# Kernel tuning notes

Hardware: AMD Instinct MI355X
Metric: run time of the kernel (lower is better)

Reference implementation:

```python
import jax, jax.numpy as jnp
import numpy as np

B, N, K, DIM = 2, 20000, 16, 256


def _mlp(x, W, b):
    # torch nn.Linear: x @ W.T + b, then LeakyReLU(0.1)
    return jax.nn.leaky_relu(x @ W.T + b, negative_slope=0.1)


def _lfa(features, geom, idx, W, b):
    # features: [B, N, C]; geom: [B, N, K, 4]; idx: [B, N, K]
    t = _mlp(geom, W, b)                                  # [B, N, K, d_lfa]
    fn = jax.vmap(lambda f, i: f[i])(features, idx)       # gather neighbors: [B, N, K, C]
    # mean over K of concat == concat of means (faithful, avoids big concat)
    return jnp.concatenate([t.mean(axis=2), fn.mean(axis=2)], axis=-1)


def _linear_init(key, out_f, in_f):
    k1, k2 = jax.random.split(key)
    bound = 1.0 / np.sqrt(in_f)
    W = jax.random.uniform(k1, (out_f, in_f), jnp.float32, -bound, bound)
    b = jax.random.uniform(k2, (out_f,), jnp.float32, -bound, bound)
    return W, b


def setup_inputs() -> dict:
    key = jax.random.key(0)
    ks = jax.random.split(key, 8)
    W_init, b_init = _linear_init(ks[0], DIM // 4, DIM)
    W_l1, b_l1 = _linear_init(ks[1], DIM // 4, 4)
    W_l2, b_l2 = _linear_init(ks[2], DIM // 2, 4)
    W_fin, b_fin = _linear_init(ks[3], DIM, DIM)
    W_id, b_id = _linear_init(ks[4], DIM, DIM)
    return {
        "input_tensor": jax.random.normal(ks[5], (B, N, DIM), jnp.float32),
        "geometric_features": jax.random.normal(ks[6], (B, N, K, 4), jnp.float32),
        "neighbor_indices": jax.random.randint(ks[7], (B, N, K), 0, N, jnp.int64 if jax.config.jax_enable_x64 else jnp.int32),
        "W_init": W_init, "b_init": b_init,
        "W_l1": W_l1, "b_l1": b_l1,
        "W_l2": W_l2, "b_l2": b_l2,
        "W_fin": W_fin, "b_fin": b_fin,
        "W_id": W_id, "b_id": b_id,
    }


def reference(input_tensor, geometric_features, neighbor_indices,
              W_init, b_init, W_l1, b_l1, W_l2, b_l2,
              W_fin, b_fin, W_id, b_id):
    residual = input_tensor
    x = _mlp(input_tensor, W_init, b_init)                       # [B, N, dim/4]
    x = _lfa(x, geometric_features, neighbor_indices, W_l1, b_l1)  # [B, N, dim/2]
    x = _lfa(x, geometric_features, neighbor_indices, W_l2, b_l2)  # [B, N, dim]
    x = _mlp(x, W_fin, b_fin)
    return x + _mlp(residual, W_id, b_id)
```

## Files before the change

kernel.cpp:

```cpp
#include <hip/hip_runtime.h>
#include <hip/hip_bf16.h>

#define BN   40000
#define NPTS 20000
#define KNN  16
#define DIM  256

typedef __attribute__((ext_vector_type(8))) short bf16x8;
typedef __attribute__((ext_vector_type(4))) float f32x4;

__device__ __forceinline__ float lrelu(float v) { return v > 0.f ? v : 0.1f * v; }
__device__ __forceinline__ float bs2f(short s) {
    union { unsigned u; float f; } c; c.u = ((unsigned)(unsigned short)s) << 16;
    return c.f;
}
__device__ __forceinline__ short f2bs(float f) {
    __hip_bfloat16 h = __float2bfloat16(f);
    return *reinterpret_cast<short*>(&h);
}
__device__ __forceinline__ bf16x8 ldf32_bf16x8(const float* p) {
    const float4 a = ((const float4*)p)[0];
    const float4 b = ((const float4*)p)[1];
    bf16x8 r;
    r[0]=f2bs(a.x); r[1]=f2bs(a.y); r[2]=f2bs(a.z); r[3]=f2bs(a.w);
    r[4]=f2bs(b.x); r[5]=f2bs(b.y); r[6]=f2bs(b.z); r[7]=f2bs(b.w);
    return r;
}

__device__ __forceinline__ void dma16(const void* g, void* l) {
    __builtin_amdgcn_global_load_lds(
        (const __attribute__((address_space(1))) unsigned int*)g,
        (__attribute__((address_space(3))) unsigned int*)l, 16, 0, 0);
}

__global__ void __launch_bounds__(256) geom_kernel(
    const float* __restrict__ geom,
    const float* __restrict__ W1, const float* __restrict__ B1,
    const float* __restrict__ W2, const float* __restrict__ B2,
    const int* __restrict__ idxw, int* __restrict__ flag,
    const float* __restrict__ Wf, const float* __restrict__ Wi,
    const float* __restrict__ Wn,
    short* __restrict__ Wt, short* __restrict__ Wnt,
    __hip_bfloat16* __restrict__ x2,
    __hip_bfloat16* __restrict__ x3)
{
    if (blockIdx.x >= 3751) {
        int t = (blockIdx.x - 3751) * 256 + threadIdx.x;
        if (t < 32768) {
            int mat = (t >> 14) & 1;
            int tt  = t & 16383;
            float4 v = mat ? ((const float4*)Wi)[tt] : ((const float4*)Wf)[tt];
            int n  = tt >> 6;
            int k  = (tt & 63) * 4;
            int kk = k >> 5, q = (k >> 3) & 3, j = k & 7;
            short4 o; o.x=f2bs(v.x); o.y=f2bs(v.y); o.z=f2bs(v.z); o.w=f2bs(v.w);
            *(short4*)(Wt + ((size_t)((kk*2 + mat)*4 + q))*2048 + n*8 + j) = o;
        } else {
            int tt = t - 32768;
            float4 v = ((const float4*)Wn)[tt];
            int n  = tt >> 6;
            int k  = (tt & 63) * 4;
            int kk = k >> 5, q = (k >> 3) & 3, j = k & 7;
            short4 o; o.x=f2bs(v.x); o.y=f2bs(v.y); o.z=f2bs(v.z); o.w=f2bs(v.w);
            *(short4*)(Wnt + ((size_t)((kk*4 + q)*64 + n))*8 + j) = o;
        }
        return;
    }
    if (blockIdx.x == 3750) {
        __shared__ int red[256];
        int t = threadIdx.x;
        int v = 0;
#pragma unroll
        for (int it = 0; it < 64; ++it)
            v |= idxw[2 * (t + it * 256) + 1];
        red[t] = v;
        __syncthreads();
        for (int s = 128; s > 0; s >>= 1) {
            if (t < s) red[t] |= red[t + s];
            __syncthreads();
        }
        if (t == 0) *flag = (red[0] != 0) ? 1 : 0;
        return;
    }
    int tid = blockIdx.x * 256 + threadIdx.x;
    int p  = tid / 24;
    int cg = tid - p * 24;
    const float4* g = (const float4*)(geom + (size_t)p * (KNN * 4));
    const float4* Wp; const float* Bp; int c0;
    if (cg < 8) { c0 = cg * 8;       Wp = (const float4*)W1; Bp = B1; }
    else        { c0 = (cg - 8) * 8; Wp = (const float4*)W2; Bp = B2; }
    float4 w[8]; float bb[8];
#pragma unroll
    for (int j = 0; j < 8; ++j) { w[j] = Wp[c0 + j]; bb[j] = Bp[c0 + j]; }
    float acc[8];
#pragma unroll
    for (int j = 0; j < 8; ++j) acc[j] = 0.f;
#pragma unroll
    for (int k = 0; k < KNN; ++k) {
        float4 gv = g[k];
#pragma unroll
        for (int j = 0; j < 8; ++j)
            acc[j] += lrelu(bb[j] + gv.x*w[j].x + gv.y*w[j].y + gv.z*w[j].z + gv.w*w[j].w);
    }
    const float s = 1.f/16.f;
    short* dst = (cg < 8) ? ((short*)x2 + (size_t)p*128 + c0)
                          : ((short*)x3 + (size_t)p*256 + c0);
    bf16x8 o;
#pragma unroll
    for (int j = 0; j < 8; ++j) o[j] = f2bs(acc[j] * s);
    *(bf16x8*)dst = o;
}

__global__ void __launch_bounds__(256) mlp_init_mfma(
    const float* __restrict__ X,
    const short* __restrict__ Wnt,
    const float* __restrict__ bias,
    __hip_bfloat16* __restrict__ Y)
{
    __shared__ short wbuf[16384];
    int t = threadIdx.x;
    int wave = t >> 6, lane = t & 63;
    int r = lane & 15, q = lane >> 4;
    {
        const char* W8 = (const char*)Wnt;
        char* L8 = (char*)wbuf;
#pragma unroll
        for (int rd = 0; rd < 8; ++rd) {
            int off = (wave * 8 + rd) * 1024 + lane * 16;
            dma16(W8 + off, L8 + off);
        }
    }
    int m0 = blockIdx.x * 64 + wave * 16;
    const float* Xs = X + (size_t)(m0 + r) * DIM + q * 8;
    bf16x8 a[8];
#pragma unroll
    for (int kk = 0; kk < 8; ++kk) a[kk] = ldf32_bf16x8(Xs + kk * 32);
    __syncthreads();

    f32x4 acc[4];
#pragma unroll
    for (int nt = 0; nt < 4; ++nt) acc[nt] = (f32x4){0.f,0.f,0.f,0.f};
#pragma unroll
    for (int kk = 0; kk < 8; ++kk) {
#pragma unroll
        for (int nt = 0; nt < 4; ++nt) {
            bf16x8 b = *(const bf16x8*)&wbuf[((kk*4 + q)*64 + nt*16 + r) * 8];
            acc[nt] = __builtin_amdgcn_mfma_f32_16x16x32_bf16(a[kk], b, acc[nt], 0, 0, 0);
        }
    }
#pragma unroll
    for (int nt = 0; nt < 4; ++nt) {
        int col = nt * 16 + r;
        float bv = bias[col];
#pragma unroll
        for (int i = 0; i < 4; ++i) {
            float v = lrelu(acc[nt][i] + bv);
            Y[(size_t)(m0 + q*4 + i) * 64 + col] = __float2bfloat16(v);
        }
    }
}

__global__ void __launch_bounds__(256) gather1_kernel(
    const int* __restrict__ idxw, const int* __restrict__ flag,
    const __hip_bfloat16* __restrict__ x1,
    __hip_bfloat16* __restrict__ x2)
{
    int t = blockIdx.x * 256 + threadIdx.x;
    int p = t >> 3, j = t & 7;
    int lane = threadIdx.x & 63;
    int dual = (*flag == 0) ? 2 : 1;
    int base = (p >= NPTS) ? NPTS : 0;
    int i0 = idxw[((size_t)p * 16 + 2*j)     * dual];
    int i1 = idxw[((size_t)p * 16 + 2*j + 1) * dual];
    int g8 = lane & 56;
    float acc[8];
#pragma unroll
    for (int i = 0; i < 8; ++i) acc[i] = 0.f;
#pragma unroll
    for (int k = 0; k < 8; ++k) {
        int rA = base + __shfl(i0, g8 + k, 64);
        int rB = base + __shfl(i1, g8 + k, 64);
        bf16x8 vA = *(const bf16x8*)((const short*)x1 + (size_t)rA * 64 + j * 8);
        bf16x8 vB = *(const bf16x8*)((const short*)x1 + (size_t)rB * 64 + j * 8);
#pragma unroll
        for (int i = 0; i < 8; ++i) acc[i] += bs2f(vA[i]) + bs2f(vB[i]);
    }
    bf16x8 o;
#pragma unroll
    for (int i = 0; i < 8; ++i) o[i] = f2bs(acc[i] * (1.f/16.f));
    *(bf16x8*)((short*)x2 + (size_t)p * 128 + 64 + j * 8) = o;
}

__global__ void __launch_bounds__(256) gather2_kernel(
    const int* __restrict__ idxw, const int* __restrict__ flag,
    const __hip_bfloat16* __restrict__ x2,
    __hip_bfloat16* __restrict__ x3)
{
    int t = blockIdx.x * 256 + threadIdx.x;
    int p = t >> 4, j = t & 15;
    int lane = threadIdx.x & 63;
    int dual = (*flag == 0) ? 2 : 1;
    int base = (p >= NPTS) ? NPTS : 0;
    int myi = idxw[((size_t)p * 16 + j) * dual];
    int g16 = lane & 48;
    float acc[8];
#pragma unroll
    for (int i = 0; i < 8; ++i) acc[i] = 0.f;
#pragma unroll
    for (int k = 0; k < KNN; ++k) {
        int row = base + __shfl(myi, g16 + k, 64);
        bf16x8 v = *(const bf16x8*)((const short*)x2 + (size_t)row * 128 + j * 8);
#pragma unroll
        for (int i = 0; i < 8; ++i) acc[i] += bs2f(v[i]);
    }
    bf16x8 o;
#pragma unroll
    for (int i = 0; i < 8; ++i) o[i] = f2bs(acc[i] * (1.f/16.f));
    *(bf16x8*)((short*)x3 + (size_t)p * 256 + 128 + j * 8) = o;
}

__global__ void __launch_bounds__(256) final_mfma(
    const __hip_bfloat16* __restrict__ X3,
    const float* __restrict__ RES,
    const short* __restrict__ Wt,
    const float* __restrict__ Bf,
    const float* __restrict__ Bi,
    float* __restrict__ OUT)
{
    __shared__ short wbuf[16384];
    int t = threadIdx.x;
    int wave = t >> 6, lane = t & 63;
    int r = lane & 15, q = lane >> 4;
    int p0 = blockIdx.x * 16;

    const char* WtB = (const char*)Wt;
    char* wbufB = (char*)wbuf;
    {
        const char* src0 = WtB + wave * 1024 + lane * 16;
#pragma unroll
        for (int rd = 0; rd < 8; ++rd)
            dma16(src0 + rd * 4096, wbufB + rd * 4096 + wave * 1024);
    }

    bf16x8 a1f[8], a2f[8];
    {
        const short* x3r = (const short*)X3 + (size_t)(p0 + r) * DIM + q * 8;
        const float* rsr = RES + (size_t)(p0 + r) * DIM + q * 8;
#pragma unroll
        for (int kk = 0; kk < 8; ++kk) {
            a1f[kk] = *(const bf16x8*)(x3r + kk * 32);
            a2f[kk] = ldf32_bf16x8(rsr + kk * 32);
        }
    }

    f32x4 acc1[4], acc2[4];
#pragma unroll
    for (int nt = 0; nt < 4; ++nt) {
        acc1[nt] = (f32x4){0.f,0.f,0.f,0.f};
        acc2[nt] = (f32x4){0.f,0.f,0.f,0.f};
    }

#pragma unroll
    for (int kk = 0; kk < 8; ++kk) {
        __syncthreads();
#pragma unroll
        for (int nt = 0; nt < 4; ++nt) {
            int n = wave * 64 + nt * 16 + r;
            bf16x8 b1 = *(const bf16x8*)&wbuf[(size_t)q * 2048 + n * 8];
            bf16x8 b2 = *(const bf16x8*)&wbuf[(size_t)(4 + q) * 2048 + n * 8];
            acc1[nt] = __builtin_amdgcn_mfma_f32_16x16x32_bf16(a1f[kk], b1, acc1[nt], 0, 0, 0);
            acc2[nt] = __builtin_amdgcn_mfma_f32_16x16x32_bf16(a2f[kk], b2, acc2[nt], 0, 0, 0);
        }
        if (kk < 7) {
            __syncthreads();
            const char* src = WtB + (size_t)(kk + 1) * 32768 + wave * 1024 + lane * 16;
#pragma unroll
            for (int rd = 0; rd < 8; ++rd)
                dma16(src + rd * 4096, wbufB + rd * 4096 + wave * 1024);
        }
    }

#pragma unroll
    for (int nt = 0; nt < 4; ++nt) {
        int col = wave * 64 + nt * 16 + r;
        float bfv = Bf[col], biv = Bi[col];
#pragma unroll
        for (int i = 0; i < 4; ++i) {
            float v = lrelu(acc1[nt][i] + bfv) + lrelu(acc2[nt][i] + biv);
            OUT[(size_t)(p0 + q*4 + i) * DIM + col] = v;
        }
    }
}

extern "C" void kernel_launch(void* const* d_in, const int* in_sizes, int n_in,
                              void* d_out, int out_size, void* d_ws, size_t ws_size,
                              hipStream_t stream)
{
    const float* input  = (const float*)d_in[0];
    const float* geom   = (const float*)d_in[1];
    const int*   idxw   = (const int*)d_in[2];
    const float* W_init = (const float*)d_in[3];
    const float* b_init = (const float*)d_in[4];
    const float* W_l1   = (const float*)d_in[5];
    const float* b_l1   = (const float*)d_in[6];
    const float* W_l2   = (const float*)d_in[7];
    const float* b_l2   = (const float*)d_in[8];
    const float* W_fin  = (const float*)d_in[9];
    const float* b_fin  = (const float*)d_in[10];
    const float* W_id   = (const float*)d_in[11];
    const float* b_id   = (const float*)d_in[12];
    float* out = (float*)d_out;

    char* ws = (char*)d_ws;
    int* flag = (int*)ws;
    short* Wt  = (short*)(ws + 16);
    short* Wnt = (short*)(ws + 16 + 262144);
    __hip_bfloat16* x2 = (__hip_bfloat16*)(ws + 16 + 5120000);
    __hip_bfloat16* x3 = (__hip_bfloat16*)(ws + 16 + 15360000);
    __hip_bfloat16* x1 = (__hip_bfloat16*)d_out;

    geom_kernel<<<3895, 256, 0, stream>>>(geom, W_l1, b_l1, W_l2, b_l2,
                                          idxw, flag, W_fin, W_id, W_init,
                                          Wt, Wnt, x2, x3);
    mlp_init_mfma<<<625, 256, 0, stream>>>(input, Wnt, b_init, x1);
    gather1_kernel<<<1250, 256, 0, stream>>>(idxw, flag, x1, x2);
    gather2_kernel<<<2500, 256, 0, stream>>>(idxw, flag, x2, x3);
    final_mfma<<<2500, 256, 0, stream>>>(x3, input, Wt, b_fin, b_id, out);
}
```

Measured before the change: 226.7 us.

## Restructure final GEMM to keep weight half resident in LDS across many rows

The final fused linear kernel now uses 512-thread blocks, each owning one half of the output columns, and loads that half of both weight matrices into 128KB of LDS once. It then loops over 320 rows in 64-row tiles instead of reloading all weights in eight staged chunks for every 16-row block. This removes repeated weight traffic and the per-chunk barriers. In exchange the grid shrinks to 250 blocks with heavy LDS use, so occupancy and parallelism drop, and each block reads its input rows for only half the output columns.

```diff
diff --git a/kernel.cpp b/kernel.cpp
--- a/kernel.cpp
+++ b/kernel.cpp
@@ -219,7 +219,7 @@
     *(bf16x8*)((short*)x3 + (size_t)p * 256 + 128 + j * 8) = o;
 }
 
-__global__ void __launch_bounds__(256) final_mfma(
+__global__ void __launch_bounds__(512, 2) final_mfma(
     const __hip_bfloat16* __restrict__ X3,
     const float* __restrict__ RES,
     const short* __restrict__ Wt,
@@ -227,67 +227,84 @@
     const float* __restrict__ Bi,
     float* __restrict__ OUT)
 {
-    __shared__ short wbuf[16384];
-    int t = threadIdx.x;
-    int wave = t >> 6, lane = t & 63;
-    int r = lane & 15, q = lane >> 4;
-    int p0 = blockIdx.x * 16;
-
-    const char* WtB = (const char*)Wt;
-    char* wbufB = (char*)wbuf;
+    __shared__ short lw[65536];
+    const int t    = threadIdx.x;
+    const int wave = t >> 6, lane = t & 63;
+    const int r = lane & 15, q = lane >> 4;
+    const int rg = wave >> 1, cg = wave & 1;
+    const int ch = blockIdx.x & 1;
+    const int p0 = (blockIdx.x >> 1) * 320;
+
     {
-        const char* src0 = WtB + wave * 1024 + lane * 16;
-#pragma unroll
-        for (int rd = 0; rd < 8; ++rd)
-            dma16(src0 + rd * 4096, wbufB + rd * 4096 + wave * 1024);
-    }
-
-    bf16x8 a1f[8], a2f[8];
-    {
-        const short* x3r = (const short*)X3 + (size_t)(p0 + r) * DIM + q * 8;
-        const float* rsr = RES + (size_t)(p0 + r) * DIM + q * 8;
+        const char* WtB = (const char*)Wt;
+        char* L = (char*)lw;
+#pragma unroll
+        for (int i = 0; i < 16; ++i) {
+            int c = wave * 8 + (i >> 1);
+            int d = i & 1;
+            int mat = c >> 5, kk = (c >> 2) & 7, qq = c & 3;
+            int src_sh = ((kk * 2 + mat) * 4 + qq) * 2048 + ch * 1024;
+            dma16(WtB + (size_t)src_sh * 2 + d * 1024 + lane * 16,
+                  L + (c * 2 + d) * 1024 + lane * 16);
+        }
+    }
+    const int cb = ch * 128 + cg * 64;
+    float bfv[4], biv[4];
+#pragma unroll
+    for (int nt = 0; nt < 4; ++nt) {
+        bfv[nt] = Bf[cb + nt * 16 + r];
+        biv[nt] = Bi[cb + nt * 16 + r];
+    }
+    __syncthreads();
+
+    const short* bpf = lw + q * 1024 + (cg * 64 + r) * 8;
+    const short* bpi = bpf + 32768;
+
+#pragma unroll
+    for (int tt = 0; tt < 5; ++tt) {
+        const int row = p0 + tt * 64 + rg * 16 + r;
+        const short* x3r = (const short*)X3 + (size_t)row * DIM + q * 8;
+        const float* rsr = RES + (size_t)row * DIM + q * 8;
+
+        bf16x8 a1[8];
+        float4 rw[16];
 #pragma unroll
         for (int kk = 0; kk < 8; ++kk) {
-            a1f[kk] = *(const bf16x8*)(x3r + kk * 32);
-            a2f[kk] = ldf32_bf16x8(rsr + kk * 32);
-        }
-    }
-
-    f32x4 acc1[4], acc2[4];
-#pragma unroll
-    for (int nt = 0; nt < 4; ++nt) {
-        acc1[nt] = (f32x4){0.f,0.f,0.f,0.f};
-        acc2[nt] = (f32x4){0.f,0.f,0.f,0.f};
-    }
-
-#pragma unroll
-    for (int kk = 0; kk < 8; ++kk) {
-        __syncthreads();
+            rw[2*kk]   = ((const float4*)rsr)[kk * 8];
+            rw[2*kk+1] = ((const float4*)rsr)[kk * 8 + 1];
+            a1[kk] = *(const bf16x8*)(x3r + kk * 32);
+        }
+
+        f32x4 acc1[4], acc2[4];
 #pragma unroll
         for (int nt = 0; nt < 4; ++nt) {
-            int n = wave * 64 + nt * 16 + r;
-            bf16x8 b1 = *(const bf16x8*)&wbuf[(size_t)q * 2048 + n * 8];
-            bf16x8 b2 = *(const bf16x8*)&wbuf[(size_t)(4 + q) * 2048 + n * 8];
-            acc1[nt] = __builtin_amdgcn_mfma_f32_16x16x32_bf16(a1f[kk], b1, acc1[nt], 0, 0, 0);
-            acc2[nt] = __builtin_amdgcn_mfma_f32_16x16x32_bf16(a2f[kk], b2, acc2[nt], 0, 0, 0);
-        }
-        if (kk < 7) {
-            __syncthreads();
-            const char* src = WtB + (size_t)(kk + 1) * 32768 + wave * 1024 + lane * 16;
-#pragma unroll
-            for (int rd = 0; rd < 8; ++rd)
-                dma16(src + rd * 4096, wbufB + rd * 4096 + wave * 1024);
-        }
-    }
-
-#pragma unroll
-    for (int nt = 0; nt < 4; ++nt) {
-        int col = wave * 64 + nt * 16 + r;
-        float bfv = Bf[col], biv = Bi[col];
-#pragma unroll
-        for (int i = 0; i < 4; ++i) {
-            float v = lrelu(acc1[nt][i] + bfv) + lrelu(acc2[nt][i] + biv);
-            OUT[(size_t)(p0 + q*4 + i) * DIM + col] = v;
+            acc1[nt] = (f32x4){0.f,0.f,0.f,0.f};
+            acc2[nt] = (f32x4){0.f,0.f,0.f,0.f};
+        }
+#pragma unroll
+        for (int kk = 0; kk < 8; ++kk) {
+            bf16x8 a2;
+            {
+                const float4 lo = rw[2*kk], hi = rw[2*kk+1];
+                a2[0]=f2bs(lo.x); a2[1]=f2bs(lo.y); a2[2]=f2bs(lo.z); a2[3]=f2bs(lo.w);
+                a2[4]=f2bs(hi.x); a2[5]=f2bs(hi.y); a2[6]=f2bs(hi.z); a2[7]=f2bs(hi.w);
+            }
+#pragma unroll
+            for (int nt = 0; nt < 4; ++nt) {
+                bf16x8 b1 = *(const bf16x8*)(bpf + kk * 4096 + nt * 128);
+                bf16x8 b2 = *(const bf16x8*)(bpi + kk * 4096 + nt * 128);
+                acc1[nt] = __builtin_amdgcn_mfma_f32_16x16x32_bf16(a1[kk], b1, acc1[nt], 0, 0, 0);
+                acc2[nt] = __builtin_amdgcn_mfma_f32_16x16x32_bf16(a2,    b2, acc2[nt], 0, 0, 0);
+            }
+        }
+#pragma unroll
+        for (int nt = 0; nt < 4; ++nt) {
+            const int col = cb + nt * 16 + r;
+#pragma unroll
+            for (int i = 0; i < 4; ++i) {
+                float v = lrelu(acc1[nt][i] + bfv[nt]) + lrelu(acc2[nt][i] + biv[nt]);
+                OUT[(size_t)(p0 + tt * 64 + rg * 16 + q * 4 + i) * DIM + col] = v;
+            }
         }
     }
 }
@@ -325,5 +342,5 @@
     mlp_init_mfma<<<625, 256, 0, stream>>>(input, Wnt, b_init, x1);
     gather1_kernel<<<1250, 256, 0, stream>>>(idxw, flag, x1, x2);
     gather2_kernel<<<2500, 256, 0, stream>>>(idxw, flag, x2, x3);
-    final_mfma<<<2500, 256, 0, stream>>>(x3, input, Wt, b_fin, b_id, out);
-}
+    final_mfma<<<250, 512, 0, stream>>>(x3, input, Wt, b_fin, b_id, out);
+}
```

Result: faster. 208.1 us (-8.2%).
